# Kernel optimization log

Measured on AMD Instinct MI355X. Metric: run time of the kernel, lower is better.

## Reference

```python
import jax, jax.numpy as jnp
import numpy as np

N, E = 100000, 1200000
IN_NF, H_NF, OUT_NF, IN_EF = 32, 64, 64, 16


def _linear_params(key, fan_in, fan_out):
    kw, kb = jax.random.split(key)
    s = 1.0 / np.sqrt(fan_in)
    W = jax.random.uniform(kw, (fan_in, fan_out), jnp.float32, -s, s)
    b = jax.random.uniform(kb, (fan_out,), jnp.float32, -s, s)
    return W, b


def setup_inputs() -> dict:
    key = jax.random.key(0)
    ks = jax.random.split(key, 16)
    inp = {
        'node_feats': jax.random.normal(ks[0], (N, IN_NF), jnp.float32),
        'edge_attr': jax.random.normal(ks[1], (E, IN_EF), jnp.float32),
        'coords': jax.random.normal(ks[2], (N, 3), jnp.float32),
        'edge_index': jax.random.randint(ks[3], (2, E), 0, N, jnp.int64),
    }
    # emb_in / emb_out
    inp['W_in'], inp['b_in'] = _linear_params(ks[4], IN_NF, H_NF)
    inp['W_out'], inp['b_out'] = _linear_params(ks[5], H_NF, OUT_NF)
    # edge MLP: cat[h_i, h_j, radial, edge_attr] -> hidden -> hidden
    edge_in = 2 * H_NF + 1 + IN_EF
    inp['We1'], inp['be1'] = _linear_params(ks[6], edge_in, H_NF)
    inp['We2'], inp['be2'] = _linear_params(ks[7], H_NF, H_NF)
    # node MLP: cat[h, agg_m] -> hidden -> out
    inp['Wn1'], inp['bn1'] = _linear_params(ks[8], H_NF + H_NF, H_NF)
    inp['Wn2'], inp['bn2'] = _linear_params(ks[9], H_NF, H_NF)
    # coord MLP: m -> hidden -> 1
    inp['Wc1'], inp['bc1'] = _linear_params(ks[10], H_NF, H_NF)
    inp['Wc2'], inp['bc2'] = _linear_params(ks[11], H_NF, 1)
    return inp


def _egnn_fwd(node_feats, edge_attr, coords, edge_index,
              W_in, b_in, We1, be1, We2, be2, Wn1, bn1, Wn2, bn2,
              Wc1, bc1, Wc2, bc2, W_out, b_out):
    relu = jax.nn.relu
    n = node_feats.shape[0]
    row, col = edge_index[0], edge_index[1]

    h = node_feats @ W_in + b_in                       # [N, H]

    # --- edge model ---
    coord_diff = coords[row] - coords[col]             # [E, 3]
    radial = jnp.sum(coord_diff * coord_diff, axis=-1, keepdims=True)  # [E, 1]
    edge_in = jnp.concatenate([h[row], h[col], radial, edge_attr], axis=-1)
    m = relu(relu(edge_in @ We1 + be1) @ We2 + be2)    # [E, H]

    # --- coord model: mean-aggregate coord_diff * phi_x(m) ---
    trans = coord_diff * (relu(m @ Wc1 + bc1) @ Wc2 + bc2)  # [E, 3]
    agg_x = jax.ops.segment_sum(trans, row, num_segments=n)
    cnt = jax.ops.segment_sum(jnp.ones((trans.shape[0],), trans.dtype), row, num_segments=n)
    coords = coords + agg_x / jnp.maximum(cnt, 1.0)[:, None]

    # --- node model: sum-aggregate messages ---
    agg_m = jax.ops.segment_sum(m, row, num_segments=n)  # [N, H]
    h = relu(jnp.concatenate([h, agg_m], axis=-1) @ Wn1 + bn1) @ Wn2 + bn2

    out = h @ W_out + b_out                            # [N, OUT]
    return out, coords


def reference(node_feats, edge_attr, coords, edge_index,
              W_in, b_in, W_out, b_out, We1, be1, We2, be2,
              Wn1, bn1, Wn2, bn2, Wc1, bc1, Wc2, bc2):
    return _egnn_fwd(node_feats, edge_attr, coords, edge_index,
                     W_in, b_in, We1, be1, We2, be2, Wn1, bn1, Wn2, bn2,
                     Wc1, bc1, Wc2, bc2, W_out, b_out)
```

## Files before the change

### kernel.cpp

```cpp
#include <hip/hip_runtime.h>


typedef __attribute__((ext_vector_type(4))) float f32x4;
typedef __attribute__((ext_vector_type(8))) short short8;

__device__ __forceinline__ void atomAddF(float* p, float v) { unsafeAtomicAdd(p, v); }

__device__ __forceinline__ unsigned short f2bf(float f) {
  unsigned int u = __builtin_bit_cast(unsigned int, f);
  unsigned int r = (u + 0x7FFFu + ((u >> 16) & 1u)) >> 16;
  return (unsigned short)r;
}
__device__ __forceinline__ float bf2f(unsigned short s) {
  unsigned int v = ((unsigned int)s) << 16;
  return __builtin_bit_cast(float, v);
}
__device__ __forceinline__ float lo_bf(unsigned int u) {
  return __builtin_bit_cast(float, u << 16);
}
__device__ __forceinline__ float hi_bf(unsigned int u) {
  return __builtin_bit_cast(float, u & 0xFFFF0000u);
}

__global__ __launch_bounds__(256) void k_prep(
    const float* __restrict__ nf, const float* __restrict__ W_in,
    const float* __restrict__ b_in, const float* __restrict__ We1,
    const float* __restrict__ be1, const float* __restrict__ Wn1,
    const float* __restrict__ bn1, const float* __restrict__ Wn2,
    const float* __restrict__ bn2, const float* __restrict__ W_out,
    const float* __restrict__ b_out, unsigned short* __restrict__ nfb,
    float* __restrict__ WA, float* __restrict__ WB, float* __restrict__ WF1,
    float* __restrict__ Wno, float* __restrict__ bSum, float* __restrict__ bn1f,
    float* __restrict__ bno, float* __restrict__ aggz, int N) {
  const int b = blockIdx.x, t = threadIdx.x;
  if (b == 0 || b == 1) {
    const float* Wsrc = (b == 0) ? We1 : (We1 + 64 * 64);
    float* dst = (b == 0) ? WA : WB;
    for (int idx = t; idx < 2048; idx += 256) {
      const int i = idx >> 6, n = idx & 63;
      float s = 0.f;
      for (int h = 0; h < 64; ++h) s = fmaf(W_in[i * 64 + h], Wsrc[h * 64 + n], s);
      dst[idx] = s;
    }
  } else if (b == 2) {
    for (int idx = t; idx < 2048; idx += 256) {
      const int i = idx >> 6, n = idx & 63;
      float s = 0.f;
      for (int h = 0; h < 64; ++h) s = fmaf(W_in[i * 64 + h], Wn1[h * 64 + n], s);
      WF1[idx] = s;
    }
    if (t < 64) {
      float s1 = bn1[t], s2 = be1[t];
      for (int h = 0; h < 64; ++h) {
        s1 = fmaf(b_in[h], Wn1[h * 64 + t], s1);
        s2 = fmaf(b_in[h], We1[h * 64 + t] + We1[(64 + h) * 64 + t], s2);
      }
      bn1f[t] = s1;
      bSum[t] = s2;
    }
  } else if (b <= 6) {
    const int base = (b - 3) * 1024;
    for (int idx = t; idx < 1024; idx += 256) {
      const int kk = (base + idx) >> 6, n = (base + idx) & 63;
      float s = 0.f;
      for (int h = 0; h < 64; ++h) s = fmaf(Wn2[kk * 64 + h], W_out[h * 64 + n], s);
      Wno[base + idx] = s;
    }
    if (b == 3 && t < 64) {
      float s = b_out[t];
      for (int h = 0; h < 64; ++h) s = fmaf(bn2[h], W_out[h * 64 + t], s);
      bno[t] = s;
    }
  } else {
    const int bid = b - 7, nb = gridDim.x - 7;
    const int tot8 = N * 8;
    for (int i = bid * 256 + t; i < tot8; i += nb * 256) {
      const f32x4 v = *reinterpret_cast<const f32x4*>(nf + (size_t)i * 4);
      ushort4 o;
      o.x = f2bf(v[0]); o.y = f2bf(v[1]); o.z = f2bf(v[2]); o.w = f2bf(v[3]);
      *reinterpret_cast<ushort4*>(nfb + (size_t)i * 4) = o;
    }
    const size_t tot = (size_t)N * 68;
    for (size_t i = (size_t)bid * 256 + t; i * 4 < tot; i += (size_t)nb * 256) {
      const size_t off = i * 4;
      if (off + 4 <= tot)
        *reinterpret_cast<float4*>(aggz + off) = make_float4(0.f, 0.f, 0.f, 0.f);
      else
        for (size_t q = off; q < tot; ++q) aggz[q] = 0.f;
    }
  }
}

__global__ __launch_bounds__(256) void k_gab(
    const float* __restrict__ nf, const float* __restrict__ WA,
    const float* __restrict__ WB, unsigned short* __restrict__ gA,
    unsigned short* __restrict__ gB, int N) {
  __shared__ float Ws[2 * 2048];
  __shared__ float nfl[4][8][36];
  for (int i = threadIdx.x; i < 2048; i += 256) {
    Ws[i] = WA[i];
    Ws[2048 + i] = WB[i];
  }
  __syncthreads();
  const int w = threadIdx.x >> 6, lane = threadIdx.x & 63;
  const int NG = (N + 7) >> 3;
  for (int ng = blockIdx.x * 4 + w; ng < NG; ng += gridDim.x * 4) {
    const int base = ng * 8;
    {
      const int nl = lane >> 3, ch = lane & 7;
      int n = base + nl;
      if (n >= N) n = N - 1;
      const f32x4 v = *reinterpret_cast<const f32x4*>(nf + (size_t)n * 32 + ch * 4);
      *reinterpret_cast<f32x4*>(&nfl[w][nl][ch * 4]) = v;
    }
    float aa[8], ab[8];
#pragma unroll
    for (int i = 0; i < 8; ++i) { aa[i] = 0.f; ab[i] = 0.f; }
    for (int k4 = 0; k4 < 8; ++k4) {
      float w0[2][4];
#pragma unroll
      for (int q = 0; q < 4; ++q) {
        w0[0][q] = Ws[(k4 * 4 + q) * 64 + lane];
        w0[1][q] = Ws[2048 + (k4 * 4 + q) * 64 + lane];
      }
#pragma unroll
      for (int i = 0; i < 8; ++i) {
        const f32x4 x = *reinterpret_cast<const f32x4*>(&nfl[w][i][k4 * 4]);
#pragma unroll
        for (int q = 0; q < 4; ++q) {
          aa[i] = fmaf(x[q], w0[0][q], aa[i]);
          ab[i] = fmaf(x[q], w0[1][q], ab[i]);
        }
      }
    }
#pragma unroll
    for (int i = 0; i < 8; ++i) {
      const int n = base + i;
      if (n < N) {
        gA[(size_t)n * 64 + lane] = f2bf(aa[i]);
        gB[(size_t)n * 64 + lane] = f2bf(ab[i]);
      }
    }
  }
}

__global__ __launch_bounds__(256) void k_hist(const int* __restrict__ eidx,
                                              int* __restrict__ deg, int E) {
  for (int e = blockIdx.x * 256 + threadIdx.x; e < E; e += gridDim.x * 256)
    atomicAdd(&deg[eidx[e]], 1);
}

__global__ __launch_bounds__(256) void k_scanA(const int* __restrict__ deg,
                                               int* __restrict__ excl,
                                               int* __restrict__ bsum, int N) {
  __shared__ int s[256];
  const int t = threadIdx.x;
  const int i = blockIdx.x * 256 + t;
  const int v = (i < N) ? deg[i] : 0;
  s[t] = v;
  __syncthreads();
#pragma unroll
  for (int off = 1; off < 256; off <<= 1) {
    int x = 0;
    if (t >= off) x = s[t - off];
    __syncthreads();
    s[t] += x;
    __syncthreads();
  }
  if (i < N) excl[i] = s[t] - v;
  if (t == 255) bsum[blockIdx.x] = s[255];
}

__global__ __launch_bounds__(256) void k_scanC(int* __restrict__ excl,
                                               const int* __restrict__ bsum,
                                               int N) {
  __shared__ int sh[256];
  const int t = threadIdx.x, b = blockIdx.x;
  int part = 0;
  for (int i = t; i < b; i += 256) part += bsum[i];
  sh[t] = part;
  __syncthreads();
#pragma unroll
  for (int off = 128; off; off >>= 1) {
    if (t < off) sh[t] += sh[t + off];
    __syncthreads();
  }
  const int add = sh[0];
  const int i = b * 256 + t;
  if (i < N) excl[i] += add;
}

__global__ __launch_bounds__(256) void k_scatter(
    const int* __restrict__ eidx, int* __restrict__ rowNext,
    unsigned long long* __restrict__ srt8, int E) {
  for (int e = blockIdx.x * 256 + threadIdx.x; e < E; e += gridDim.x * 256) {
    const int r = eidx[e];
    const int c = eidx[E + e];
    const int pos = atomicAdd(&rowNext[r], 1);
    srt8[pos] = (unsigned long long)r | ((unsigned long long)c << 18) |
                ((unsigned long long)e << 36);
  }
}

struct EdgeLds {
  unsigned short We2t[64 * 72];
  unsigned short Wc1t[64 * 72];
  unsigned short Bea[64 * 40];
  unsigned short x[4][32 * 72];
  float cd[4][32 * 4];
  int idx[4][32];
};

__global__ __launch_bounds__(256, 3) void k_edge(
    const unsigned short* __restrict__ gA, const unsigned short* __restrict__ gB,
    const float* __restrict__ ea, const float* __restrict__ co,
    const unsigned long long* __restrict__ srt8, const float* __restrict__ We1,
    const float* __restrict__ bSum, const float* __restrict__ be2,
    const float* __restrict__ We2, const float* __restrict__ bc1,
    const float* __restrict__ Wc1, const float* __restrict__ Wc2,
    const float* __restrict__ bc2, float* __restrict__ agg_m,
    float* __restrict__ agg_x, int E) {
  __shared__ EdgeLds S;
  const int tid = threadIdx.x;
  for (int i = tid; i < 4096; i += 256) {
    const int k = i >> 6, n = i & 63;
    S.We2t[n * 72 + k] = f2bf(We2[k * 64 + n]);
    S.Wc1t[n * 72 + k] = f2bf(Wc1[k * 64 + n]);
  }
  for (int i = tid; i < 2048; i += 256) {
    const int k = i >> 6, n = i & 63;
    const float v = (k < 16) ? We1[(129 + k) * 64 + n]
                             : ((k == 16) ? We1[128 * 64 + n] : 0.f);
    S.Bea[n * 40 + k] = f2bf(v);
  }
  __syncthreads();

  const int w = tid >> 6, lane = tid & 63;
  const int g = lane >> 4, t = lane & 15;
  const float bc2v = bc2[0];

  float bS_r[4], be2_r[4], bc1_r[4], wc2_r[4];
#pragma unroll
  for (int nt = 0; nt < 4; ++nt) {
    const int n = t + 16 * nt;
    bS_r[nt] = bSum[n];
    be2_r[nt] = be2[n];
    bc1_r[nt] = bc1[n];
    wc2_r[nt] = Wc2[n];
  }

  unsigned short* xw = &S.x[w][0];
  float* cdw = &S.cd[w][0];
  int* idxw = &S.idx[w][0];
  const int ngroups = (E + 31) >> 5;

  for (int grp = blockIdx.x * 4 + w; grp < ngroups; grp += gridDim.x * 4) {
    const int e0 = grp * 32;
    unsigned long long s8 = 0;
    if (lane < 32) {
      int e = e0 + lane;
      if (e >= E) e = E - 1;
      s8 = srt8[e];
    }
    const int r_dec = (int)(s8 & 0x3FFFFull);
    const int c_dec = (int)((s8 >> 18) & 0x3FFFFull);
    const int p_dec = (int)(s8 >> 36);
    if (lane < 32) idxw[lane] = r_dec;

    const int el0 = lane & 31;
    const int rE = __shfl(r_dec, el0, 64);
    const int cE = __shfl(c_dec, el0, 64);
    if (lane < 32) {
      const float dx = co[(size_t)rE * 3 + 0] - co[(size_t)cE * 3 + 0];
      const float dy = co[(size_t)rE * 3 + 1] - co[(size_t)cE * 3 + 1];
      const float dz = co[(size_t)rE * 3 + 2] - co[(size_t)cE * 3 + 2];
      f32x4 c4;
      c4[0] = dx; c4[1] = dy; c4[2] = dz; c4[3] = dx * dx + dy * dy + dz * dz;
      *reinterpret_cast<f32x4*>(&cdw[el0 * 4]) = c4;
    }

#pragma unroll
    for (int rr = 0; rr < 4; ++rr) {
      const int el = rr * 8 + (lane >> 3), ch = lane & 7;
      const int rI = __shfl(r_dec, el, 64);
      const int cI = __shfl(c_dec, el, 64);
      const uint4 va = *reinterpret_cast<const uint4*>(gA + (size_t)rI * 64 + ch * 8);
      const uint4 vb = *reinterpret_cast<const uint4*>(gB + (size_t)cI * 64 + ch * 8);
      const unsigned int a[4] = {va.x, va.y, va.z, va.w};
      const unsigned int b[4] = {vb.x, vb.y, vb.z, vb.w};
      uint4 o;
      unsigned int r[4];
#pragma unroll
      for (int q = 0; q < 4; ++q) {
        const float s0 = lo_bf(a[q]) + lo_bf(b[q]);
        const float s1 = hi_bf(a[q]) + hi_bf(b[q]);
        r[q] = ((unsigned int)f2bf(s1) << 16) | (unsigned int)f2bf(s0);
      }
      o.x = r[0]; o.y = r[1]; o.z = r[2]; o.w = r[3];
      *reinterpret_cast<uint4*>(&xw[el * 72 + ch * 8]) = o;
    }

    short8 a1[2];
#pragma unroll
    for (int mt = 0; mt < 2; ++mt) {
      const int eaI = __shfl(p_dec, t + 16 * mt, 64);
      short8 a = {};
      if (g < 2) {
        const float* pe2 = ea + (size_t)eaI * 16 + g * 8;
        const f32x4 x0 = *reinterpret_cast<const f32x4*>(pe2);
        const f32x4 x1 = *reinterpret_cast<const f32x4*>(pe2 + 4);
#pragma unroll
        for (int q = 0; q < 4; ++q) {
          a[q] = (short)f2bf(x0[q]);
          a[4 + q] = (short)f2bf(x1[q]);
        }
      } else if (g == 2) {
        a[0] = (short)f2bf(cdw[(t + 16 * mt) * 4 + 3]);
      }
      a1[mt] = a;
    }

    f32x4 acc[2][4];
#pragma unroll
    for (int mt = 0; mt < 2; ++mt)
#pragma unroll
      for (int nt = 0; nt < 4; ++nt)
#pragma unroll
        for (int j = 0; j < 4; ++j) {
          const int row = g * 4 + j + 16 * mt, col = t + 16 * nt;
          acc[mt][nt][j] = bf2f(xw[row * 72 + col]) + bS_r[nt];
        }
#pragma unroll
    for (int mt = 0; mt < 2; ++mt)
#pragma unroll
      for (int nt = 0; nt < 4; ++nt) {
        const short8 b = *reinterpret_cast<const short8*>(&S.Bea[(t + 16 * nt) * 40 + g * 8]);
        acc[mt][nt] = __builtin_amdgcn_mfma_f32_16x16x32_bf16(a1[mt], b, acc[mt][nt], 0, 0, 0);
      }
#pragma unroll
    for (int mt = 0; mt < 2; ++mt)
#pragma unroll
      for (int nt = 0; nt < 4; ++nt)
#pragma unroll
        for (int j = 0; j < 4; ++j) {
          const float v = fmaxf(acc[mt][nt][j], 0.f);
          xw[(g * 4 + j + 16 * mt) * 72 + t + 16 * nt] = f2bf(v);
        }
    short8 A2[2][2];
#pragma unroll
    for (int mt = 0; mt < 2; ++mt)
#pragma unroll
      for (int kt = 0; kt < 2; ++kt)
        A2[mt][kt] = *reinterpret_cast<const short8*>(&xw[(t + 16 * mt) * 72 + kt * 32 + g * 8]);
    f32x4 m2[2][4];
#pragma unroll
    for (int mt = 0; mt < 2; ++mt)
#pragma unroll
      for (int nt = 0; nt < 4; ++nt) {
        f32x4 c;
        c[0] = be2_r[nt]; c[1] = be2_r[nt]; c[2] = be2_r[nt]; c[3] = be2_r[nt];
#pragma unroll
        for (int kt = 0; kt < 2; ++kt) {
          const short8 b = *reinterpret_cast<const short8*>(
              &S.We2t[(t + 16 * nt) * 72 + kt * 32 + g * 8]);
          c = __builtin_amdgcn_mfma_f32_16x16x32_bf16(A2[mt][kt], b, c, 0, 0, 0);
        }
#pragma unroll
        for (int j = 0; j < 4; ++j) c[j] = fmaxf(c[j], 0.f);
        m2[mt][nt] = c;
      }
#pragma unroll
    for (int mt = 0; mt < 2; ++mt)
#pragma unroll
      for (int nt = 0; nt < 4; ++nt)
#pragma unroll
        for (int j = 0; j < 4; ++j)
          xw[(g * 4 + j + 16 * mt) * 72 + t + 16 * nt] = f2bf(m2[mt][nt][j]);

    short8 A3[2][2];
#pragma unroll
    for (int mt = 0; mt < 2; ++mt)
#pragma unroll
      for (int kt = 0; kt < 2; ++kt)
        A3[mt][kt] = *reinterpret_cast<const short8*>(&xw[(t + 16 * mt) * 72 + kt * 32 + g * 8]);
    float sv[2][4];
#pragma unroll
    for (int mt = 0; mt < 2; ++mt)
#pragma unroll
      for (int j = 0; j < 4; ++j) sv[mt][j] = 0.f;
#pragma unroll
    for (int mt = 0; mt < 2; ++mt)
#pragma unroll
      for (int nt = 0; nt < 4; ++nt) {
        f32x4 c;
        c[0] = bc1_r[nt]; c[1] = bc1_r[nt]; c[2] = bc1_r[nt]; c[3] = bc1_r[nt];
#pragma unroll
        for (int kt = 0; kt < 2; ++kt) {
          const short8 b = *reinterpret_cast<const short8*>(
              &S.Wc1t[(t + 16 * nt) * 72 + kt * 32 + g * 8]);
          c = __builtin_amdgcn_mfma_f32_16x16x32_bf16(A3[mt][kt], b, c, 0, 0, 0);
        }
#pragma unroll
        for (int j = 0; j < 4; ++j) sv[mt][j] = fmaf(fmaxf(c[j], 0.f), wc2_r[nt], sv[mt][j]);
      }
#pragma unroll
    for (int d = 1; d < 16; d <<= 1)
#pragma unroll
      for (int mt = 0; mt < 2; ++mt)
#pragma unroll
        for (int j = 0; j < 4; ++j) sv[mt][j] += __shfl_xor(sv[mt][j], d, 64);
#pragma unroll
    for (int mt = 0; mt < 2; ++mt)
#pragma unroll
      for (int j = 0; j < 4; ++j) sv[mt][j] += bc2v;

#pragma unroll
    for (int mt = 0; mt < 2; ++mt)
#pragma unroll
      for (int j = 0; j < 4; ++j)
        if (t == 0) cdw[(g * 4 + j + 16 * mt) * 4 + 3] = sv[mt][j];

    {
      float accm = 0.f;
#pragma unroll
      for (int r = 0; r < 32; ++r) {
        const int rIr = idxw[r];
        const bool valid = (e0 + r) < E;
        if (valid) accm += bf2f(xw[r * 72 + lane]);
        const bool closes = (r == 31) || ((e0 + r + 1) >= E) || (idxw[r + 1] != rIr);
        if (valid && closes) {
          atomAddF(&agg_m[(size_t)rIr * 64 + lane], accm);
          accm = 0.f;
        }
      }
    }
    if (lane < 3) {
      float accx = 0.f;
#pragma unroll
      for (int r = 0; r < 32; ++r) {
        const int rIr = idxw[r];
        const bool valid = (e0 + r) < E;
        if (valid) accx += cdw[r * 4 + lane] * cdw[r * 4 + 3];
        const bool closes = (r == 31) || ((e0 + r + 1) >= E) || (idxw[r + 1] != rIr);
        if (valid && closes) {
          atomAddF(&agg_x[(size_t)rIr * 3 + lane], accx);
          accx = 0.f;
        }
      }
    }
  }
}

struct NodeLds {
  unsigned short Wn1bT[64 * 72];
  unsigned short WnoT[64 * 72];
  unsigned short x[4][32 * 72];
};

__global__ __launch_bounds__(256, 4) void k_node(
    const unsigned short* __restrict__ nfb, const float* __restrict__ agg_m,
    const float* __restrict__ agg_x, const int* __restrict__ deg,
    const float* __restrict__ co, const float* __restrict__ WF1,
    const float* __restrict__ Wn1, const float* __restrict__ Wno,
    const float* __restrict__ bn1f, const float* __restrict__ bno,
    float* __restrict__ out, float* __restrict__ co_out, int N) {
  __shared__ NodeLds S;
  const int tid = threadIdx.x;
  for (int i = tid; i < 4096; i += 256) {
    const int k = i >> 6, n = i & 63;
    S.Wn1bT[n * 72 + k] = f2bf(Wn1[(64 + k) * 64 + n]);
    S.WnoT[n * 72 + k] = f2bf(Wno[k * 64 + n]);
  }
  __syncthreads();
  const int w = tid >> 6, lane = tid & 63;
  const int g = lane >> 4, t = lane & 15;

  short8 fW1[4];
  float b1_r[4], bo_r[4];
#pragma unroll
  for (int nt = 0; nt < 4; ++nt) {
    const int n = t + 16 * nt;
    short8 a;
#pragma unroll
    for (int j = 0; j < 8; ++j) a[j] = (short)f2bf(WF1[(g * 8 + j) * 64 + n]);
    fW1[nt] = a;
    b1_r[nt] = bn1f[n];
    bo_r[nt] = bno[n];
  }

  unsigned short* xw = &S.x[w][0];
  const int ngroups = (N + 31) >> 5;
  const int GS = gridDim.x * 4;

  for (int grp = blockIdx.x * 4 + w; grp < ngroups; grp += GS) {
    const int base = grp * 32;
    short8 A1[2], Aa[2][2];
#pragma unroll
    for (int mt = 0; mt < 2; ++mt) {
      int node = base + t + 16 * mt;
      if (node >= N) node = N - 1;
      A1[mt] = *reinterpret_cast<const short8*>(nfb + (size_t)node * 32 + g * 8);
#pragma unroll
      for (int kt = 0; kt < 2; ++kt) {
        const f32x4 v0 = *reinterpret_cast<const f32x4*>(
            agg_m + (size_t)node * 64 + kt * 32 + g * 8);
        const f32x4 v1 = *reinterpret_cast<const f32x4*>(
            agg_m + (size_t)node * 64 + kt * 32 + g * 8 + 4);
        short8 a;
#pragma unroll
        for (int j = 0; j < 4; ++j) {
          a[j] = (short)f2bf(v0[j]);
          a[4 + j] = (short)f2bf(v1[j]);
        }
        Aa[mt][kt] = a;
      }
    }
    f32x4 acc[2][4];
#pragma unroll
    for (int mt = 0; mt < 2; ++mt)
#pragma unroll
      for (int nt = 0; nt < 4; ++nt) {
        const int n = t + 16 * nt;
        f32x4 c;
        c[0] = b1_r[nt]; c[1] = b1_r[nt]; c[2] = b1_r[nt]; c[3] = b1_r[nt];
        c = __builtin_amdgcn_mfma_f32_16x16x32_bf16(A1[mt], fW1[nt], c, 0, 0, 0);
#pragma unroll
        for (int kt = 0; kt < 2; ++kt) {
          const short8 b = *reinterpret_cast<const short8*>(
              &S.Wn1bT[n * 72 + kt * 32 + g * 8]);
          c = __builtin_amdgcn_mfma_f32_16x16x32_bf16(Aa[mt][kt], b, c, 0, 0, 0);
        }
        acc[mt][nt] = c;
      }
#pragma unroll
    for (int mt = 0; mt < 2; ++mt)
#pragma unroll
      for (int nt = 0; nt < 4; ++nt)
#pragma unroll
        for (int j = 0; j < 4; ++j)
          xw[(g * 4 + j + 16 * mt) * 72 + t + 16 * nt] =
              f2bf(fmaxf(acc[mt][nt][j], 0.f));
    short8 A2[2][2];
#pragma unroll
    for (int mt = 0; mt < 2; ++mt)
#pragma unroll
      for (int kt = 0; kt < 2; ++kt)
        A2[mt][kt] = *reinterpret_cast<const short8*>(
            &S.x[w][(t + 16 * mt) * 72 + kt * 32 + g * 8]);
#pragma unroll
    for (int mt = 0; mt < 2; ++mt)
#pragma unroll
      for (int nt = 0; nt < 4; ++nt) {
        const int n = t + 16 * nt;
        f32x4 c;
        c[0] = bo_r[nt]; c[1] = bo_r[nt]; c[2] = bo_r[nt]; c[3] = bo_r[nt];
#pragma unroll
        for (int kt = 0; kt < 2; ++kt) {
          const short8 b = *reinterpret_cast<const short8*>(
              &S.WnoT[n * 72 + kt * 32 + g * 8]);
          c = __builtin_amdgcn_mfma_f32_16x16x32_bf16(A2[mt][kt], b, c, 0, 0, 0);
        }
#pragma unroll
        for (int j = 0; j < 4; ++j) {
          const int node = base + g * 4 + j + 16 * mt;
          if (node < N) out[(size_t)node * 64 + n] = c[j];
        }
      }
    if (lane < 32) {
      const int node = base + lane;
      if (node < N) {
        const float dv = fmaxf((float)deg[node], 1.f);
#pragma unroll
        for (int d = 0; d < 3; ++d)
          co_out[(size_t)node * 3 + d] =
              co[(size_t)node * 3 + d] + agg_x[(size_t)node * 3 + d] / dv;
      }
    }
  }
}

extern "C" void kernel_launch(void* const* d_in, const int* in_sizes, int n_in,
                              void* d_out, int out_size, void* d_ws, size_t ws_size,
                              hipStream_t stream) {
  const float* nf = (const float*)d_in[0];
  const float* ea = (const float*)d_in[1];
  const float* co = (const float*)d_in[2];
  const int* ei = (const int*)d_in[3];
  const float* W_in = (const float*)d_in[4];
  const float* b_in = (const float*)d_in[5];
  const float* W_out = (const float*)d_in[6];
  const float* b_out = (const float*)d_in[7];
  const float* We1 = (const float*)d_in[8];
  const float* be1 = (const float*)d_in[9];
  const float* We2 = (const float*)d_in[10];
  const float* be2 = (const float*)d_in[11];
  const float* Wn1 = (const float*)d_in[12];
  const float* bn1 = (const float*)d_in[13];
  const float* Wn2 = (const float*)d_in[14];
  const float* bn2 = (const float*)d_in[15];
  const float* Wc1 = (const float*)d_in[16];
  const float* bc1 = (const float*)d_in[17];
  const float* Wc2 = (const float*)d_in[18];
  const float* bc2 = (const float*)d_in[19];

  const int N = in_sizes[0] / 32;
  const int E = in_sizes[1] / 16;

  float* ws = (float*)d_ws;
  float* agg_m = ws;
  float* agg_x = agg_m + (size_t)N * 64;
  int* deg = (int*)(agg_x + (size_t)N * 3);
  float* WA = (float*)(deg + N);
  float* WB = WA + 2048;
  float* WF1 = WB + 2048;
  float* Wno = WF1 + 2048;
  float* bSum = Wno + 4096;
  float* bn1f = bSum + 64;
  float* bno = bn1f + 64;
  int* rowNext = (int*)(bno + 64);
  int* bsumBuf = rowNext + N;
  uintptr_t pp = (uintptr_t)(bsumBuf + 512);
  pp = (pp + 7) & ~(uintptr_t)7;
  unsigned long long* srt8 = (unsigned long long*)pp;
  unsigned short* nfb = (unsigned short*)(srt8 + E);

  float* outp = (float*)d_out;
  float* co_out = outp + (size_t)N * 64;
  unsigned short* gA = (unsigned short*)d_out;
  unsigned short* gB = gA + (size_t)N * 64;

  const int nb = (N + 255) / 256;

  k_prep<<<1031, 256, 0, stream>>>(nf, W_in, b_in, We1, be1, Wn1, bn1, Wn2,
                                   bn2, W_out, b_out, nfb, WA, WB, WF1, Wno,
                                   bSum, bn1f, bno, agg_m, N);
  k_gab<<<2048, 256, 0, stream>>>(nf, WA, WB, gA, gB, N);
  k_hist<<<512, 256, 0, stream>>>(ei, deg, E);
  k_scanA<<<nb, 256, 0, stream>>>(deg, rowNext, bsumBuf, N);
  k_scanC<<<nb, 256, 0, stream>>>(rowNext, bsumBuf, N);
  k_scatter<<<512, 256, 0, stream>>>(ei, rowNext, srt8, E);
  k_edge<<<768, 256, 0, stream>>>(gA, gB, ea, co, srt8, We1, bSum, be2, We2,
                                  bc1, Wc1, Wc2, bc2, agg_m, agg_x, E);
  k_node<<<1024, 256, 0, stream>>>(nfb, agg_m, agg_x, deg, co, WF1, Wn1, Wno,
                                   bn1f, bno, outp, co_out, N);
}
```

Measured before the change: 424.5 us.

## Fuse node projection into prep kernel and swizzle edge-kernel LDS layout

Folds the separate k_gab launch into k_prep. Each worker block now recomputes the W_in·We1 folded weights into shared memory, converts node features to bf16 in the same pass, and adds the combined bias into gA instead of in the edge kernel. The edge kernel drops the padded LDS rows in favour of XOR-swizzled 128-byte rows and shrinks the edge-attr weight tile, which cuts LDS use enough to raise occupancy to 4 blocks per CU with a larger grid. The cost is that each of ~1024 prep blocks redundantly computes a 32x64x64 weight product before starting useful work.

Result: slower. 781.4 us (+84.1%).

```diff
diff --git a/kernel.cpp b/kernel.cpp
--- a/kernel.cpp
+++ b/kernel.cpp
@@ -29,20 +29,11 @@
     const float* __restrict__ bn1, const float* __restrict__ Wn2,
     const float* __restrict__ bn2, const float* __restrict__ W_out,
     const float* __restrict__ b_out, unsigned short* __restrict__ nfb,
-    float* __restrict__ WA, float* __restrict__ WB, float* __restrict__ WF1,
-    float* __restrict__ Wno, float* __restrict__ bSum, float* __restrict__ bn1f,
+    unsigned short* __restrict__ gA, unsigned short* __restrict__ gB,
+    float* __restrict__ WF1, float* __restrict__ Wno, float* __restrict__ bn1f,
     float* __restrict__ bno, float* __restrict__ aggz, int N) {
   const int b = blockIdx.x, t = threadIdx.x;
-  if (b == 0 || b == 1) {
-    const float* Wsrc = (b == 0) ? We1 : (We1 + 64 * 64);
-    float* dst = (b == 0) ? WA : WB;
-    for (int idx = t; idx < 2048; idx += 256) {
-      const int i = idx >> 6, n = idx & 63;
-      float s = 0.f;
-      for (int h = 0; h < 64; ++h) s = fmaf(W_in[i * 64 + h], Wsrc[h * 64 + n], s);
-      dst[idx] = s;
-    }
-  } else if (b == 2) {
+  if (b == 0) {
     for (int idx = t; idx < 2048; idx += 256) {
       const int i = idx >> 6, n = idx & 63;
       float s = 0.f;
@@ -50,95 +41,99 @@
       WF1[idx] = s;
     }
     if (t < 64) {
-      float s1 = bn1[t], s2 = be1[t];
-      for (int h = 0; h < 64; ++h) {
-        s1 = fmaf(b_in[h], Wn1[h * 64 + t], s1);
-        s2 = fmaf(b_in[h], We1[h * 64 + t] + We1[(64 + h) * 64 + t], s2);
-      }
+      float s1 = bn1[t];
+      for (int h = 0; h < 64; ++h) s1 = fmaf(b_in[h], Wn1[h * 64 + t], s1);
       bn1f[t] = s1;
-      bSum[t] = s2;
-    }
-  } else if (b <= 6) {
-    const int base = (b - 3) * 1024;
+    }
+  } else if (b <= 4) {
+    const int base = (b - 1) * 1024;
     for (int idx = t; idx < 1024; idx += 256) {
       const int kk = (base + idx) >> 6, n = (base + idx) & 63;
       float s = 0.f;
       for (int h = 0; h < 64; ++h) s = fmaf(Wn2[kk * 64 + h], W_out[h * 64 + n], s);
       Wno[base + idx] = s;
     }
-    if (b == 3 && t < 64) {
+    if (b == 1 && t < 64) {
       float s = b_out[t];
       for (int h = 0; h < 64; ++h) s = fmaf(bn2[h], W_out[h * 64 + t], s);
       bno[t] = s;
     }
   } else {
-    const int bid = b - 7, nb = gridDim.x - 7;
-    const int tot8 = N * 8;
-    for (int i = bid * 256 + t; i < tot8; i += nb * 256) {
-      const f32x4 v = *reinterpret_cast<const f32x4*>(nf + (size_t)i * 4);
-      ushort4 o;
-      o.x = f2bf(v[0]); o.y = f2bf(v[1]); o.z = f2bf(v[2]); o.w = f2bf(v[3]);
-      *reinterpret_cast<ushort4*>(nfb + (size_t)i * 4) = o;
-    }
-    const size_t tot = (size_t)N * 68;
-    for (size_t i = (size_t)bid * 256 + t; i * 4 < tot; i += (size_t)nb * 256) {
-      const size_t off = i * 4;
-      if (off + 4 <= tot)
-        *reinterpret_cast<float4*>(aggz + off) = make_float4(0.f, 0.f, 0.f, 0.f);
-      else
-        for (size_t q = off; q < tot; ++q) aggz[q] = 0.f;
-    }
-  }
-}
-
-__global__ __launch_bounds__(256) void k_gab(
-    const float* __restrict__ nf, const float* __restrict__ WA,
-    const float* __restrict__ WB, unsigned short* __restrict__ gA,
-    unsigned short* __restrict__ gB, int N) {
-  __shared__ float Ws[2 * 2048];
-  __shared__ float nfl[4][8][36];
-  for (int i = threadIdx.x; i < 2048; i += 256) {
-    Ws[i] = WA[i];
-    Ws[2048 + i] = WB[i];
-  }
-  __syncthreads();
-  const int w = threadIdx.x >> 6, lane = threadIdx.x & 63;
-  const int NG = (N + 7) >> 3;
-  for (int ng = blockIdx.x * 4 + w; ng < NG; ng += gridDim.x * 4) {
-    const int base = ng * 8;
+    __shared__ float WAs[2048], WBs[2048];
+    __shared__ float bSumL[64];
+    __shared__ float nfl[4][8][36];
+    for (int idx = t; idx < 2048; idx += 256) {
+      const int i = idx >> 6, n = idx & 63;
+      float sa = 0.f, sb = 0.f;
+      for (int h = 0; h < 64; ++h) {
+        const float wv = W_in[i * 64 + h];
+        sa = fmaf(wv, We1[h * 64 + n], sa);
+        sb = fmaf(wv, We1[(64 + h) * 64 + n], sb);
+      }
+      WAs[idx] = sa;
+      WBs[idx] = sb;
+    }
+    if (t < 64) {
+      float s2 = be1[t];
+      for (int h = 0; h < 64; ++h)
+        s2 = fmaf(b_in[h], We1[h * 64 + t] + We1[(64 + h) * 64 + t], s2);
+      bSumL[t] = s2;
+    }
+    __syncthreads();
+
+    const int bid = b - 5, nbk = gridDim.x - 5;
     {
-      const int nl = lane >> 3, ch = lane & 7;
-      int n = base + nl;
-      if (n >= N) n = N - 1;
-      const f32x4 v = *reinterpret_cast<const f32x4*>(nf + (size_t)n * 32 + ch * 4);
-      *reinterpret_cast<f32x4*>(&nfl[w][nl][ch * 4]) = v;
-    }
-    float aa[8], ab[8];
-#pragma unroll
-    for (int i = 0; i < 8; ++i) { aa[i] = 0.f; ab[i] = 0.f; }
-    for (int k4 = 0; k4 < 8; ++k4) {
-      float w0[2][4];
-#pragma unroll
-      for (int q = 0; q < 4; ++q) {
-        w0[0][q] = Ws[(k4 * 4 + q) * 64 + lane];
-        w0[1][q] = Ws[2048 + (k4 * 4 + q) * 64 + lane];
+      const size_t tot = (size_t)N * 68;
+      for (size_t i = (size_t)bid * 256 + t; i * 4 < tot; i += (size_t)nbk * 256) {
+        const size_t off = i * 4;
+        if (off + 4 <= tot)
+          *reinterpret_cast<float4*>(aggz + off) = make_float4(0.f, 0.f, 0.f, 0.f);
+        else
+          for (size_t q = off; q < tot; ++q) aggz[q] = 0.f;
+      }
+    }
+    const int w = t >> 6, lane = t & 63;
+    const float bS = bSumL[lane];
+    const int NG = (N + 7) >> 3;
+    for (int ng = bid * 4 + w; ng < NG; ng += nbk * 4) {
+      const int base = ng * 8;
+      {
+        const int nl = lane >> 3, ch = lane & 7;
+        int n = base + nl;
+        if (n >= N) n = N - 1;
+        const f32x4 v = *reinterpret_cast<const f32x4*>(nf + (size_t)n * 32 + ch * 4);
+        *reinterpret_cast<f32x4*>(&nfl[w][nl][ch * 4]) = v;
+        ushort4 o;
+        o.x = f2bf(v[0]); o.y = f2bf(v[1]); o.z = f2bf(v[2]); o.w = f2bf(v[3]);
+        *reinterpret_cast<ushort4*>(nfb + (size_t)n * 32 + ch * 4) = o;
+      }
+      float aa[8], ab[8];
+#pragma unroll
+      for (int i = 0; i < 8; ++i) { aa[i] = bS; ab[i] = 0.f; }
+      for (int k4 = 0; k4 < 8; ++k4) {
+        float w0[2][4];
+#pragma unroll
+        for (int q = 0; q < 4; ++q) {
+          w0[0][q] = WAs[(k4 * 4 + q) * 64 + lane];
+          w0[1][q] = WBs[(k4 * 4 + q) * 64 + lane];
+        }
+#pragma unroll
+        for (int i = 0; i < 8; ++i) {
+          const f32x4 x = *reinterpret_cast<const f32x4*>(&nfl[w][i][k4 * 4]);
+#pragma unroll
+          for (int q = 0; q < 4; ++q) {
+            aa[i] = fmaf(x[q], w0[0][q], aa[i]);
+            ab[i] = fmaf(x[q], w0[1][q], ab[i]);
+          }
+        }
       }
 #pragma unroll
       for (int i = 0; i < 8; ++i) {
-        const f32x4 x = *reinterpret_cast<const f32x4*>(&nfl[w][i][k4 * 4]);
-#pragma unroll
-        for (int q = 0; q < 4; ++q) {
-          aa[i] = fmaf(x[q], w0[0][q], aa[i]);
-          ab[i] = fmaf(x[q], w0[1][q], ab[i]);
-        }
-      }
-    }
-#pragma unroll
-    for (int i = 0; i < 8; ++i) {
-      const int n = base + i;
-      if (n < N) {
-        gA[(size_t)n * 64 + lane] = f2bf(aa[i]);
-        gB[(size_t)n * 64 + lane] = f2bf(ab[i]);
+        const int n = base + i;
+        if (n < N) {
+          gA[(size_t)n * 64 + lane] = f2bf(aa[i]);
+          gB[(size_t)n * 64 + lane] = f2bf(ab[i]);
+        }
       }
     }
   }
@@ -203,35 +198,37 @@
 }
 
 struct EdgeLds {
-  unsigned short We2t[64 * 72];
-  unsigned short Wc1t[64 * 72];
-  unsigned short Bea[64 * 40];
-  unsigned short x[4][32 * 72];
+  unsigned short We2t[4096];
+  unsigned short Wc1t[4096];
+  unsigned short WeaP[64 * 24];
+  unsigned short x[4][32 * 64];
   float cd[4][32 * 4];
   int idx[4][32];
 };
 
-__global__ __launch_bounds__(256, 3) void k_edge(
+__global__ __launch_bounds__(256, 4) void k_edge(
     const unsigned short* __restrict__ gA, const unsigned short* __restrict__ gB,
     const float* __restrict__ ea, const float* __restrict__ co,
     const unsigned long long* __restrict__ srt8, const float* __restrict__ We1,
-    const float* __restrict__ bSum, const float* __restrict__ be2,
-    const float* __restrict__ We2, const float* __restrict__ bc1,
-    const float* __restrict__ Wc1, const float* __restrict__ Wc2,
-    const float* __restrict__ bc2, float* __restrict__ agg_m,
-    float* __restrict__ agg_x, int E) {
+    const float* __restrict__ be2, const float* __restrict__ We2,
+    const float* __restrict__ bc1, const float* __restrict__ Wc1,
+    const float* __restrict__ Wc2, const float* __restrict__ bc2,
+    float* __restrict__ agg_m, float* __restrict__ agg_x, int E) {
   __shared__ EdgeLds S;
   const int tid = threadIdx.x;
   for (int i = tid; i < 4096; i += 256) {
     const int k = i >> 6, n = i & 63;
-    S.We2t[n * 72 + k] = f2bf(We2[k * 64 + n]);
-    S.Wc1t[n * 72 + k] = f2bf(Wc1[k * 64 + n]);
-  }
-  for (int i = tid; i < 2048; i += 256) {
-    const int k = i >> 6, n = i & 63;
+    const int byt = n * 128 + ((k * 2) ^ ((n & 7) << 4));
+    *reinterpret_cast<unsigned short*>(reinterpret_cast<char*>(S.We2t) + byt) =
+        f2bf(We2[k * 64 + n]);
+    *reinterpret_cast<unsigned short*>(reinterpret_cast<char*>(S.Wc1t) + byt) =
+        f2bf(Wc1[k * 64 + n]);
+  }
+  for (int i = tid; i < 64 * 24; i += 256) {
+    const int n = i / 24, k = i - n * 24;
     const float v = (k < 16) ? We1[(129 + k) * 64 + n]
                              : ((k == 16) ? We1[128 * 64 + n] : 0.f);
-    S.Bea[n * 40 + k] = f2bf(v);
+    S.WeaP[n * 24 + k] = f2bf(v);
   }
   __syncthreads();
 
@@ -239,17 +236,16 @@
   const int g = lane >> 4, t = lane & 15;
   const float bc2v = bc2[0];
 
-  float bS_r[4], be2_r[4], bc1_r[4], wc2_r[4];
+  float be2_r[4], bc1_r[4], wc2_r[4];
 #pragma unroll
   for (int nt = 0; nt < 4; ++nt) {
     const int n = t + 16 * nt;
-    bS_r[nt] = bSum[n];
     be2_r[nt] = be2[n];
     bc1_r[nt] = bc1[n];
     wc2_r[nt] = Wc2[n];
   }
 
-  unsigned short* xw = &S.x[w][0];
+  char* xb = reinterpret_cast<char*>(&S.x[w][0]);
   float* cdw = &S.cd[w][0];
   int* idxw = &S.idx[w][0];
   const int ngroups = (E + 31) >> 5;
@@ -297,7 +293,7 @@
         r[q] = ((unsigned int)f2bf(s1) << 16) | (unsigned int)f2bf(s0);
       }
       o.x = r[0]; o.y = r[1]; o.z = r[2]; o.w = r[3];
-      *reinterpret_cast<uint4*>(&xw[el * 72 + ch * 8]) = o;
+      *reinterpret_cast<uint4*>(xb + el * 128 + ((ch * 16) ^ ((el & 7) << 4))) = o;
     }
 
     short8 a1[2];
@@ -328,13 +324,19 @@
 #pragma unroll
         for (int j = 0; j < 4; ++j) {
           const int row = g * 4 + j + 16 * mt, col = t + 16 * nt;
-          acc[mt][nt][j] = bf2f(xw[row * 72 + col]) + bS_r[nt];
+          acc[mt][nt][j] = bf2f(*reinterpret_cast<const unsigned short*>(
+              xb + row * 128 + ((col * 2) ^ ((row & 7) << 4))));
         }
 #pragma unroll
     for (int mt = 0; mt < 2; ++mt)
 #pragma unroll
       for (int nt = 0; nt < 4; ++nt) {
-        const short8 b = *reinterpret_cast<const short8*>(&S.Bea[(t + 16 * nt) * 40 + g * 8]);
+        const int n = t + 16 * nt;
+        short8 b = {};
+        if (g < 2)
+          b = *reinterpret_cast<const short8*>(&S.WeaP[n * 24 + g * 8]);
+        else if (g == 2)
+          b[0] = (short)S.WeaP[n * 24 + 16];
         acc[mt][nt] = __builtin_amdgcn_mfma_f32_16x16x32_bf16(a1[mt], b, acc[mt][nt], 0, 0, 0);
       }
 #pragma unroll
@@ -343,26 +345,33 @@
       for (int nt = 0; nt < 4; ++nt)
 #pragma unroll
         for (int j = 0; j < 4; ++j) {
-          const float v = fmaxf(acc[mt][nt][j], 0.f);
-          xw[(g * 4 + j + 16 * mt) * 72 + t + 16 * nt] = f2bf(v);
+          const int row = g * 4 + j + 16 * mt, col = t + 16 * nt;
+          *reinterpret_cast<unsigned short*>(
+              xb + row * 128 + ((col * 2) ^ ((row & 7) << 4))) =
+              f2bf(fmaxf(acc[mt][nt][j], 0.f));
         }
     short8 A2[2][2];
 #pragma unroll
     for (int mt = 0; mt < 2; ++mt)
 #pragma unroll
-      for (int kt = 0; kt < 2; ++kt)
-        A2[mt][kt] = *reinterpret_cast<const short8*>(&xw[(t + 16 * mt) * 72 + kt * 32 + g * 8]);
+      for (int kt = 0; kt < 2; ++kt) {
+        const int row = t + 16 * mt;
+        A2[mt][kt] = *reinterpret_cast<const short8*>(
+            xb + row * 128 + ((kt * 64 + g * 16) ^ ((row & 7) << 4)));
+      }
     f32x4 m2[2][4];
 #pragma unroll
     for (int mt = 0; mt < 2; ++mt)
 #pragma unroll
       for (int nt = 0; nt < 4; ++nt) {
+        const int n = t + 16 * nt;
         f32x4 c;
         c[0] = be2_r[nt]; c[1] = be2_r[nt]; c[2] = be2_r[nt]; c[3] = be2_r[nt];
 #pragma unroll
         for (int kt = 0; kt < 2; ++kt) {
           const short8 b = *reinterpret_cast<const short8*>(
-              &S.We2t[(t + 16 * nt) * 72 + kt * 32 + g * 8]);
+              reinterpret_cast<char*>(S.We2t) + n * 128 +
+              ((kt * 64 + g * 16) ^ ((n & 7) << 4)));
           c = __builtin_amdgcn_mfma_f32_16x16x32_bf16(A2[mt][kt], b, c, 0, 0, 0);
         }
 #pragma unroll
@@ -374,15 +383,21 @@
 #pragma unroll
       for (int nt = 0; nt < 4; ++nt)
 #pragma unroll
-        for (int j = 0; j < 4; ++j)
-          xw[(g * 4 + j + 16 * mt) * 72 + t + 16 * nt] = f2bf(m2[mt][nt][j]);
-
+        for (int j = 0; j < 4; ++j) {
+          const int row = g * 4 + j + 16 * mt, col = t + 16 * nt;
+          *reinterpret_cast<unsigned short*>(
+              xb + row * 128 + ((col * 2) ^ ((row & 7) << 4))) =
+              f2bf(m2[mt][nt][j]);
+        }
     short8 A3[2][2];
 #pragma unroll
     for (int mt = 0; mt < 2; ++mt)
 #pragma unroll
-      for (int kt = 0; kt < 2; ++kt)
-        A3[mt][kt] = *reinterpret_cast<const short8*>(&xw[(t + 16 * mt) * 72 + kt * 32 + g * 8]);
+      for (int kt = 0; kt < 2; ++kt) {
+        const int row = t + 16 * mt;
+        A3[mt][kt] = *reinterpret_cast<const short8*>(
+            xb + row * 128 + ((kt * 64 + g * 16) ^ ((row & 7) << 4)));
+      }
     float sv[2][4];
 #pragma unroll
     for (int mt = 0; mt < 2; ++mt)
@@ -392,12 +407,14 @@
     for (int mt = 0; mt < 2; ++mt)
 #pragma unroll
       for (int nt = 0; nt < 4; ++nt) {
+        const int n = t + 16 * nt;
         f32x4 c;
         c[0] = bc1_r[nt]; c[1] = bc1_r[nt]; c[2] = bc1_r[nt]; c[3] = bc1_r[nt];
 #pragma unroll
         for (int kt = 0; kt < 2; ++kt) {
           const short8 b = *reinterpret_cast<const short8*>(
-              &S.Wc1t[(t + 16 * nt) * 72 + kt * 32 + g * 8]);
+              reinterpret_cast<char*>(S.Wc1t) + n * 128 +
+              ((kt * 64 + g * 16) ^ ((n & 7) << 4)));
           c = __builtin_amdgcn_mfma_f32_16x16x32_bf16(A3[mt][kt], b, c, 0, 0, 0);
         }
 #pragma unroll
@@ -413,7 +430,6 @@
     for (int mt = 0; mt < 2; ++mt)
 #pragma unroll
       for (int j = 0; j < 4; ++j) sv[mt][j] += bc2v;
-
 #pragma unroll
     for (int mt = 0; mt < 2; ++mt)
 #pragma unroll
@@ -426,7 +442,9 @@
       for (int r = 0; r < 32; ++r) {
         const int rIr = idxw[r];
         const bool valid = (e0 + r) < E;
-        if (valid) accm += bf2f(xw[r * 72 + lane]);
+        const float mv = bf2f(*reinterpret_cast<const unsigned short*>(
+            xb + r * 128 + ((lane * 2) ^ ((r & 7) << 4))));
+        if (valid) accm += mv;
         const bool closes = (r == 31) || ((e0 + r + 1) >= E) || (idxw[r + 1] != rIr);
         if (valid && closes) {
           atomAddF(&agg_m[(size_t)rIr * 64 + lane], accm);
@@ -610,12 +628,9 @@
   float* agg_m = ws;
   float* agg_x = agg_m + (size_t)N * 64;
   int* deg = (int*)(agg_x + (size_t)N * 3);
-  float* WA = (float*)(deg + N);
-  float* WB = WA + 2048;
-  float* WF1 = WB + 2048;
+  float* WF1 = (float*)(deg + N);
   float* Wno = WF1 + 2048;
-  float* bSum = Wno + 4096;
-  float* bn1f = bSum + 64;
+  float* bn1f = Wno + 4096;
   float* bno = bn1f + 64;
   int* rowNext = (int*)(bno + 64);
   int* bsumBuf = rowNext + N;
@@ -631,16 +646,15 @@
 
   const int nb = (N + 255) / 256;
 
-  k_prep<<<1031, 256, 0, stream>>>(nf, W_in, b_in, We1, be1, Wn1, bn1, Wn2,
-                                   bn2, W_out, b_out, nfb, WA, WB, WF1, Wno,
-                                   bSum, bn1f, bno, agg_m, N);
-  k_gab<<<2048, 256, 0, stream>>>(nf, WA, WB, gA, gB, N);
+  k_prep<<<1029, 256, 0, stream>>>(nf, W_in, b_in, We1, be1, Wn1, bn1, Wn2,
+                                   bn2, W_out, b_out, nfb, gA, gB, WF1, Wno,
+                                   bn1f, bno, agg_m, N);
   k_hist<<<512, 256, 0, stream>>>(ei, deg, E);
   k_scanA<<<nb, 256, 0, stream>>>(deg, rowNext, bsumBuf, N);
   k_scanC<<<nb, 256, 0, stream>>>(rowNext, bsumBuf, N);
   k_scatter<<<512, 256, 0, stream>>>(ei, rowNext, srt8, E);
-  k_edge<<<768, 256, 0, stream>>>(gA, gB, ea, co, srt8, We1, bSum, be2, We2,
-                                  bc1, Wc1, Wc2, bc2, agg_m, agg_x, E);
+  k_edge<<<1024, 256, 0, stream>>>(gA, gB, ea, co, srt8, We1, be2, We2, bc1,
+                                   Wc1, Wc2, bc2, agg_m, agg_x, E);
   k_node<<<1024, 256, 0, stream>>>(nfb, agg_m, agg_x, deg, co, WF1, Wn1, Wno,
                                    bn1f, bno, outp, co_out, N);
 }
```
